# Kernel optimization log

Hardware: AMD Instinct MI355X
Metric: run time of the kernel (lower is better)

## Reference

```python
import jax, jax.numpy as jnp
import numpy as np

SHRINK_THRES = 0.0025
EPS = 1e-12  # F.normalize default eps


def _l2norm(v, axis=-1):
    return v / jnp.maximum(jnp.linalg.norm(v, axis=axis, keepdims=True), EPS)


def setup_inputs() -> dict:
    key = jax.random.key(0)
    ks = jax.random.split(key, 5)
    N, C, H, W = 16, 256, 64, 64
    mem_dim = 512
    x = jax.random.normal(ks[0], (N, C, H, W), dtype=jnp.float32)
    memory = jax.random.normal(ks[1], (mem_dim, C), dtype=jnp.float32) * 0.1
    memory = _l2norm(memory, axis=1)
    w1 = jax.random.normal(ks[2], (C, C // 2), dtype=jnp.float32) * (1.0 / np.sqrt(C))
    b1 = jnp.zeros((C // 2,), dtype=jnp.float32)
    w2 = jax.random.normal(ks[3], (C // 2, C), dtype=jnp.float32) * (1.0 / np.sqrt(C // 2))
    b2 = jnp.zeros((C,), dtype=jnp.float32)
    return {"x": x, "memory": memory, "w1": w1, "b1": b1, "w2": w2, "b2": b2}


def reference(x, memory, w1, b1, w2, b2):
    N, C, H, W = x.shape
    # [N,C,H,W] -> [N*H*W, C]
    x_flat = jnp.transpose(x, (0, 2, 3, 1)).reshape(-1, C)
    x_norm = _l2norm(x_flat, axis=1)
    # shared MLP over memory slots: Linear -> ReLU -> Linear -> ReLU
    m = jax.nn.relu(memory @ w1 + b1)
    m = jax.nn.relu(m @ w2 + b2)
    mem_norm = _l2norm(m, axis=1)  # [M, C]
    # cosine similarity + softmax over memory slots
    att = jax.nn.softmax(x_norm @ mem_norm.T, axis=1)  # [N*H*W, M]
    # hard shrink + L1 renormalization
    att = jax.nn.relu(att - SHRINK_THRES)
    att = att / jnp.maximum(jnp.sum(att, axis=1, keepdims=True), EPS)
    out_flat = att @ mem_norm  # [N*H*W, C]
    output = jnp.transpose(out_flat.reshape(N, H, W, C), (0, 3, 1, 2))
    att_map = jnp.transpose(att.reshape(N, H, W, -1), (0, 3, 1, 2))
    return output, att_map
```

## Files before the change

kernel.cpp:

```cpp
#include <hip/hip_runtime.h>
#include <hip/hip_bf16.h>

typedef _Float16 half8 __attribute__((ext_vector_type(8)));
typedef _Float16 half4v __attribute__((ext_vector_type(4)));
typedef float floatx4 __attribute__((ext_vector_type(4)));

#define C_DIM 256
#define M_DIM 512
#define HW 4096
#define TAU 0.0025f

__global__ __launch_bounds__(128) void prep_kernel(
    const float* __restrict__ memory, const float* __restrict__ w1,
    const float* __restrict__ b1, const float* __restrict__ w2,
    const float* __restrict__ b2,
    _Float16* __restrict__ mNh, _Float16* __restrict__ mNl,
    _Float16* __restrict__ mNt)
{
  __shared__ float sm[256];
  __shared__ float sh[128];
  __shared__ float s_part[2];
  __shared__ float s_tot;
  const int r = blockIdx.x;
  const int t = threadIdx.x;
  sm[t]       = memory[r * C_DIM + t];
  sm[t + 128] = memory[r * C_DIM + t + 128];
  __syncthreads();
  float acc = b1[t];
#pragma unroll 8
  for (int c = 0; c < 256; ++c) acc = fmaf(sm[c], w1[c * 128 + t], acc);
  sh[t] = fmaxf(acc, 0.f);
  __syncthreads();
  float o0 = b2[t], o1 = b2[t + 128];
#pragma unroll 8
  for (int k = 0; k < 128; ++k) {
    float h = sh[k];
    o0 = fmaf(h, w2[k * 256 + t], o0);
    o1 = fmaf(h, w2[k * 256 + t + 128], o1);
  }
  o0 = fmaxf(o0, 0.f);
  o1 = fmaxf(o1, 0.f);
  float ss = o0 * o0 + o1 * o1;
#pragma unroll
  for (int off = 32; off >= 1; off >>= 1) ss += __shfl_down(ss, off);
  if ((t & 63) == 0) s_part[t >> 6] = ss;
  __syncthreads();
  if (t == 0) s_tot = s_part[0] + s_part[1];
  __syncthreads();
  const float inv = 1.f / fmaxf(sqrtf(s_tot), 1e-12f);
  const float v0 = o0 * inv, v1 = o1 * inv;
  const _Float16 h0 = (_Float16)v0, h1 = (_Float16)v1;
  mNh[r * C_DIM + t]        = h0;
  mNh[r * C_DIM + t + 128]  = h1;
  mNl[r * C_DIM + t]        = (_Float16)(v0 - (float)h0);
  mNl[r * C_DIM + t + 128]  = (_Float16)(v1 - (float)h1);
  mNt[t * M_DIM + r]        = h0;
  mNt[(t + 128) * M_DIM + r] = h1;
}

__global__ __launch_bounds__(512, 2) void main_kernel(
    const float* __restrict__ x,
    const _Float16* __restrict__ mNh, const _Float16* __restrict__ mNl,
    const _Float16* __restrict__ mNt,
    float* __restrict__ out, float* __restrict__ attmap)
{
  __shared__ _Float16 Xh[64][264];
  __shared__ _Float16 Xl[64][264];
  __shared__ _Float16 attb[64][520];
  __shared__ float s_red[64][8];
  __shared__ float s_stat[64];
  __shared__ float s_inv[64];
  __shared__ float s_sumsq[64];

  const int tid  = threadIdx.x;
  const int wave = tid >> 6;
  const int lane = tid & 63;
  const int q    = lane >> 4;
  const int c16  = lane & 15;
  const int px   = tid & 63;
  const int g    = tid >> 6;

  const int blk = blockIdx.x;
  const int img = blk >> 6;
  const int hw0 = (blk & 63) * 64;
  const float* __restrict__ xb = x + (size_t)img * C_DIM * HW + hw0;

  if (tid < 64) s_sumsq[tid] = 0.f;
  __syncthreads();

  float part = 0.f;
#pragma unroll
  for (int i = 0; i < 8; ++i) {
    const int cb = i * 32 + g * 4;
    const float v0 = xb[(size_t)(cb + 0) * HW + px];
    const float v1 = xb[(size_t)(cb + 1) * HW + px];
    const float v2 = xb[(size_t)(cb + 2) * HW + px];
    const float v3 = xb[(size_t)(cb + 3) * HW + px];
    part += v0 * v0 + v1 * v1 + v2 * v2 + v3 * v3;
    const _Float16 h0 = (_Float16)v0, h1 = (_Float16)v1, h2 = (_Float16)v2, h3 = (_Float16)v3;
    half4v hv = {h0, h1, h2, h3};
    half4v lv = {(_Float16)(v0 - (float)h0), (_Float16)(v1 - (float)h1),
                 (_Float16)(v2 - (float)h2), (_Float16)(v3 - (float)h3)};
    *(half4v*)&Xh[px][cb] = hv;
    *(half4v*)&Xl[px][cb] = lv;
  }
  atomicAdd(&s_sumsq[px], part);
  __syncthreads();
  if (tid < 64) s_inv[tid] = 1.f / fmaxf(sqrtf(s_sumsq[tid]), 1e-12f);
  __syncthreads();

  floatx4 acc[4][4];
#pragma unroll
  for (int mt = 0; mt < 4; ++mt)
#pragma unroll
    for (int nt = 0; nt < 4; ++nt) {
      floatx4 z = {0.f, 0.f, 0.f, 0.f};
      acc[mt][nt] = z;
    }

#pragma unroll
  for (int kb = 0; kb < 8; ++kb) {
    const int k0 = kb * 32 + q * 8;
    half8 ah[4], al[4];
#pragma unroll
    for (int mt = 0; mt < 4; ++mt) {
      ah[mt] = *(const half8*)&Xh[mt * 16 + c16][k0];
      al[mt] = *(const half8*)&Xl[mt * 16 + c16][k0];
    }
#pragma unroll
    for (int nt = 0; nt < 4; ++nt) {
      const int n = wave * 64 + nt * 16 + c16;
      const half8 bh = *(const half8*)(mNh + (size_t)n * C_DIM + k0);
      const half8 bl = *(const half8*)(mNl + (size_t)n * C_DIM + k0);
#pragma unroll
      for (int mt = 0; mt < 4; ++mt) {
        acc[mt][nt] = __builtin_amdgcn_mfma_f32_16x16x32_f16(ah[mt], bh, acc[mt][nt], 0, 0, 0);
        acc[mt][nt] = __builtin_amdgcn_mfma_f32_16x16x32_f16(ah[mt], bl, acc[mt][nt], 0, 0, 0);
        acc[mt][nt] = __builtin_amdgcn_mfma_f32_16x16x32_f16(al[mt], bh, acc[mt][nt], 0, 0, 0);
      }
    }
  }

#pragma unroll
  for (int mt = 0; mt < 4; ++mt)
#pragma unroll
    for (int r = 0; r < 4; ++r) {
      const float iv = s_inv[mt * 16 + q * 4 + r];
#pragma unroll
      for (int nt = 0; nt < 4; ++nt) acc[mt][nt][r] *= iv;
    }

#pragma unroll
  for (int mt = 0; mt < 4; ++mt)
#pragma unroll
    for (int r = 0; r < 4; ++r) {
      float v = fmaxf(fmaxf(acc[mt][0][r], acc[mt][1][r]), fmaxf(acc[mt][2][r], acc[mt][3][r]));
      v = fmaxf(v, __shfl_xor(v, 1));
      v = fmaxf(v, __shfl_xor(v, 2));
      v = fmaxf(v, __shfl_xor(v, 4));
      v = fmaxf(v, __shfl_xor(v, 8));
      if (c16 == 0) s_red[mt * 16 + q * 4 + r][wave] = v;
    }
  __syncthreads();
  if (tid < 64) {
    float v = s_red[tid][0];
#pragma unroll
    for (int w = 1; w < 8; ++w) v = fmaxf(v, s_red[tid][w]);
    s_stat[tid] = v;
  }
  __syncthreads();

#pragma unroll
  for (int mt = 0; mt < 4; ++mt)
#pragma unroll
    for (int r = 0; r < 4; ++r) {
      const float mx = s_stat[mt * 16 + q * 4 + r];
      float s = 0.f;
#pragma unroll
      for (int nt = 0; nt < 4; ++nt) {
        const float e = __expf(acc[mt][nt][r] - mx);
        acc[mt][nt][r] = e;
        s += e;
      }
      s += __shfl_xor(s, 1);
      s += __shfl_xor(s, 2);
      s += __shfl_xor(s, 4);
      s += __shfl_xor(s, 8);
      if (c16 == 0) s_red[mt * 16 + q * 4 + r][wave] = s;
    }
  __syncthreads();
  if (tid < 64) {
    float v = 0.f;
#pragma unroll
    for (int w = 0; w < 8; ++w) v += s_red[tid][w];
    s_stat[tid] = 1.f / v;
  }
  __syncthreads();

#pragma unroll
  for (int mt = 0; mt < 4; ++mt)
#pragma unroll
    for (int r = 0; r < 4; ++r) {
      const float isum = s_stat[mt * 16 + q * 4 + r];
      float s = 0.f;
#pragma unroll
      for (int nt = 0; nt < 4; ++nt) {
        const float tv = fmaxf(acc[mt][nt][r] * isum - TAU, 0.f);
        acc[mt][nt][r] = tv;
        s += tv;
      }
      s += __shfl_xor(s, 1);
      s += __shfl_xor(s, 2);
      s += __shfl_xor(s, 4);
      s += __shfl_xor(s, 8);
      if (c16 == 0) s_red[mt * 16 + q * 4 + r][wave] = s;
    }
  __syncthreads();
  if (tid < 64) {
    float v = 0.f;
#pragma unroll
    for (int w = 0; w < 8; ++w) v += s_red[tid][w];
    s_stat[tid] = 1.f / fmaxf(v, 1e-12f);
  }
  __syncthreads();

#pragma unroll
  for (int mt = 0; mt < 4; ++mt)
#pragma unroll
    for (int r = 0; r < 4; ++r) {
      const int m = mt * 16 + q * 4 + r;
      const float rs = s_stat[m];
#pragma unroll
      for (int nt = 0; nt < 4; ++nt)
        attb[m][wave * 64 + nt * 16 + c16] = (_Float16)(acc[mt][nt][r] * rs);
    }
  __syncthreads();

#pragma unroll
  for (int i = 0; i < 16; ++i) {
    const int n0 = (g + 8 * i) * 4;
    const half4v v = *(const half4v*)&attb[px][n0];
    float* dst = attmap + ((size_t)img * M_DIM + n0) * HW + hw0 + px;
    dst[0]            = (float)v[0];
    dst[(size_t)HW]   = (float)v[1];
    dst[(size_t)2*HW] = (float)v[2];
    dst[(size_t)3*HW] = (float)v[3];
  }

  floatx4 acc2[4][2];
#pragma unroll
  for (int mt = 0; mt < 4; ++mt)
#pragma unroll
    for (int ct = 0; ct < 2; ++ct) {
      floatx4 z = {0.f, 0.f, 0.f, 0.f};
      acc2[mt][ct] = z;
    }
#pragma unroll
  for (int kb = 0; kb < 16; ++kb) {
    const int k0 = kb * 32 + q * 8;
    half8 a[4];
#pragma unroll
    for (int mt = 0; mt < 4; ++mt) a[mt] = *(const half8*)&attb[mt * 16 + c16][k0];
#pragma unroll
    for (int ct = 0; ct < 2; ++ct) {
      const int cc = wave * 32 + ct * 16 + c16;
      const half8 b = *(const half8*)(mNt + (size_t)cc * M_DIM + k0);
#pragma unroll
      for (int mt = 0; mt < 4; ++mt)
        acc2[mt][ct] = __builtin_amdgcn_mfma_f32_16x16x32_f16(a[mt], b, acc2[mt][ct], 0, 0, 0);
    }
  }

#pragma unroll
  for (int mt = 0; mt < 4; ++mt)
#pragma unroll
    for (int ct = 0; ct < 2; ++ct)
#pragma unroll
      for (int r = 0; r < 4; ++r)
        Xh[mt * 16 + q * 4 + r][wave * 32 + ct * 16 + c16] = (_Float16)acc2[mt][ct][r];
  __syncthreads();
#pragma unroll
  for (int i = 0; i < 8; ++i) {
    const int c0 = (g + 8 * i) * 4;
    const half4v v = *(const half4v*)&Xh[px][c0];
    float* dst = out + ((size_t)img * C_DIM + c0) * HW + hw0 + px;
    dst[0]            = (float)v[0];
    dst[(size_t)HW]   = (float)v[1];
    dst[(size_t)2*HW] = (float)v[2];
    dst[(size_t)3*HW] = (float)v[3];
  }
}

extern "C" void kernel_launch(void* const* d_in, const int* in_sizes, int n_in,
                              void* d_out, int out_size, void* d_ws, size_t ws_size,
                              hipStream_t stream) {
  (void)in_sizes; (void)n_in; (void)out_size; (void)ws_size;
  const float* x      = (const float*)d_in[0];
  const float* memory = (const float*)d_in[1];
  const float* w1     = (const float*)d_in[2];
  const float* b1     = (const float*)d_in[3];
  const float* w2     = (const float*)d_in[4];
  const float* b2     = (const float*)d_in[5];
  float* out    = (float*)d_out;
  float* attmap = out + (size_t)16 * C_DIM * HW;

  _Float16* mNh = (_Float16*)d_ws;
  _Float16* mNl = mNh + (size_t)M_DIM * C_DIM;
  _Float16* mNt = mNl + (size_t)M_DIM * C_DIM;

  hipLaunchKernelGGL(prep_kernel, dim3(M_DIM), dim3(128), 0, stream,
                     memory, w1, b1, w2, b2, mNh, mNl, mNt);
  hipLaunchKernelGGL(main_kernel, dim3(1024), dim3(512), 0, stream,
                     x, mNh, mNl, mNt, out, attmap);
}
```

Baseline: 395.6 us.

## Drop split-fp16 GEMM, skip softmax max, shrink tiles and alias shared memory

Removes the hi/lo fp16 split for x and memory, so the similarity GEMM uses one MFMA per tile instead of three. Drops the softmax max-subtraction pass, relying on cosine similarity being bounded in [-1,1]. Halves the pixel tile to 32 per block, doubling the grid, and aliases the X, attention and output buffers in one shared array so more blocks fit per CU (launch bounds raised). Output is staged as fp32 instead of fp16. The main risk is accuracy, since x is now only fp16 precision in the first GEMM.

```diff
diff --git a/kernel.cpp b/kernel.cpp
--- a/kernel.cpp
+++ b/kernel.cpp
@@ -14,8 +14,7 @@
     const float* __restrict__ memory, const float* __restrict__ w1,
     const float* __restrict__ b1, const float* __restrict__ w2,
     const float* __restrict__ b2,
-    _Float16* __restrict__ mNh, _Float16* __restrict__ mNl,
-    _Float16* __restrict__ mNt)
+    _Float16* __restrict__ mN, _Float16* __restrict__ mNt)
 {
   __shared__ float sm[256];
   __shared__ float sh[128];
@@ -50,68 +49,61 @@
   const float inv = 1.f / fmaxf(sqrtf(s_tot), 1e-12f);
   const float v0 = o0 * inv, v1 = o1 * inv;
   const _Float16 h0 = (_Float16)v0, h1 = (_Float16)v1;
-  mNh[r * C_DIM + t]        = h0;
-  mNh[r * C_DIM + t + 128]  = h1;
-  mNl[r * C_DIM + t]        = (_Float16)(v0 - (float)h0);
-  mNl[r * C_DIM + t + 128]  = (_Float16)(v1 - (float)h1);
+  mN[r * C_DIM + t]         = h0;
+  mN[r * C_DIM + t + 128]   = h1;
   mNt[t * M_DIM + r]        = h0;
   mNt[(t + 128) * M_DIM + r] = h1;
 }
 
-__global__ __launch_bounds__(512, 2) void main_kernel(
+__global__ __launch_bounds__(512, 6) void main_kernel(
     const float* __restrict__ x,
-    const _Float16* __restrict__ mNh, const _Float16* __restrict__ mNl,
+    const _Float16* __restrict__ mN,
     const _Float16* __restrict__ mNt,
     float* __restrict__ out, float* __restrict__ attmap)
 {
-  __shared__ _Float16 Xh[64][264];
-  __shared__ _Float16 Xl[64][264];
-  __shared__ _Float16 attb[64][520];
-  __shared__ float s_red[64][8];
-  __shared__ float s_stat[64];
-  __shared__ float s_inv[64];
-  __shared__ float s_sumsq[64];
+  __shared__ __align__(16) unsigned char smem_u[33280];
+  __shared__ float s_red[32][8];
+  __shared__ float s_stat[32];
+  __shared__ float s_sumsq[32];
+
+  _Float16 (*Xh)[264]   = (_Float16(*)[264])smem_u;
+  _Float16 (*attb)[520] = (_Float16(*)[520])smem_u;
+  float    (*Ost)[260]  = (float(*)[260])smem_u;
 
   const int tid  = threadIdx.x;
   const int wave = tid >> 6;
   const int lane = tid & 63;
   const int q    = lane >> 4;
   const int c16  = lane & 15;
-  const int px   = tid & 63;
-  const int g    = tid >> 6;
+  const int px   = tid & 31;
+  const int cg   = tid >> 5;
 
   const int blk = blockIdx.x;
-  const int img = blk >> 6;
-  const int hw0 = (blk & 63) * 64;
+  const int img = blk >> 7;
+  const int hw0 = (blk & 127) * 32;
   const float* __restrict__ xb = x + (size_t)img * C_DIM * HW + hw0;
 
-  if (tid < 64) s_sumsq[tid] = 0.f;
+  if (tid < 32) s_sumsq[tid] = 0.f;
   __syncthreads();
 
   float part = 0.f;
 #pragma unroll
-  for (int i = 0; i < 8; ++i) {
-    const int cb = i * 32 + g * 4;
+  for (int i = 0; i < 4; ++i) {
+    const int cb = i * 64 + cg * 4;
     const float v0 = xb[(size_t)(cb + 0) * HW + px];
     const float v1 = xb[(size_t)(cb + 1) * HW + px];
     const float v2 = xb[(size_t)(cb + 2) * HW + px];
     const float v3 = xb[(size_t)(cb + 3) * HW + px];
     part += v0 * v0 + v1 * v1 + v2 * v2 + v3 * v3;
-    const _Float16 h0 = (_Float16)v0, h1 = (_Float16)v1, h2 = (_Float16)v2, h3 = (_Float16)v3;
-    half4v hv = {h0, h1, h2, h3};
-    half4v lv = {(_Float16)(v0 - (float)h0), (_Float16)(v1 - (float)h1),
-                 (_Float16)(v2 - (float)h2), (_Float16)(v3 - (float)h3)};
+    half4v hv = {(_Float16)v0, (_Float16)v1, (_Float16)v2, (_Float16)v3};
     *(half4v*)&Xh[px][cb] = hv;
-    *(half4v*)&Xl[px][cb] = lv;
   }
   atomicAdd(&s_sumsq[px], part);
   __syncthreads();
-  if (tid < 64) s_inv[tid] = 1.f / fmaxf(sqrtf(s_sumsq[tid]), 1e-12f);
-  __syncthreads();
-
-  floatx4 acc[4][4];
-#pragma unroll
-  for (int mt = 0; mt < 4; ++mt)
+
+  floatx4 acc[2][4];
+#pragma unroll
+  for (int mt = 0; mt < 2; ++mt)
 #pragma unroll
     for (int nt = 0; nt < 4; ++nt) {
       floatx4 z = {0.f, 0.f, 0.f, 0.f};
@@ -121,64 +113,29 @@
 #pragma unroll
   for (int kb = 0; kb < 8; ++kb) {
     const int k0 = kb * 32 + q * 8;
-    half8 ah[4], al[4];
-#pragma unroll
-    for (int mt = 0; mt < 4; ++mt) {
-      ah[mt] = *(const half8*)&Xh[mt * 16 + c16][k0];
-      al[mt] = *(const half8*)&Xl[mt * 16 + c16][k0];
-    }
+    half8 ah[2];
+#pragma unroll
+    for (int mt = 0; mt < 2; ++mt) ah[mt] = *(const half8*)&Xh[mt * 16 + c16][k0];
 #pragma unroll
     for (int nt = 0; nt < 4; ++nt) {
       const int n = wave * 64 + nt * 16 + c16;
-      const half8 bh = *(const half8*)(mNh + (size_t)n * C_DIM + k0);
-      const half8 bl = *(const half8*)(mNl + (size_t)n * C_DIM + k0);
-#pragma unroll
-      for (int mt = 0; mt < 4; ++mt) {
+      const half8 bh = *(const half8*)(mN + (size_t)n * C_DIM + k0);
+#pragma unroll
+      for (int mt = 0; mt < 2; ++mt)
         acc[mt][nt] = __builtin_amdgcn_mfma_f32_16x16x32_f16(ah[mt], bh, acc[mt][nt], 0, 0, 0);
-        acc[mt][nt] = __builtin_amdgcn_mfma_f32_16x16x32_f16(ah[mt], bl, acc[mt][nt], 0, 0, 0);
-        acc[mt][nt] = __builtin_amdgcn_mfma_f32_16x16x32_f16(al[mt], bh, acc[mt][nt], 0, 0, 0);
-      }
-    }
-  }
-
-#pragma unroll
-  for (int mt = 0; mt < 4; ++mt)
+    }
+  }
+
+#pragma unroll
+  for (int mt = 0; mt < 2; ++mt)
 #pragma unroll
     for (int r = 0; r < 4; ++r) {
-      const float iv = s_inv[mt * 16 + q * 4 + r];
-#pragma unroll
-      for (int nt = 0; nt < 4; ++nt) acc[mt][nt][r] *= iv;
-    }
-
-#pragma unroll
-  for (int mt = 0; mt < 4; ++mt)
-#pragma unroll
-    for (int r = 0; r < 4; ++r) {
-      float v = fmaxf(fmaxf(acc[mt][0][r], acc[mt][1][r]), fmaxf(acc[mt][2][r], acc[mt][3][r]));
-      v = fmaxf(v, __shfl_xor(v, 1));
-      v = fmaxf(v, __shfl_xor(v, 2));
-      v = fmaxf(v, __shfl_xor(v, 4));
-      v = fmaxf(v, __shfl_xor(v, 8));
-      if (c16 == 0) s_red[mt * 16 + q * 4 + r][wave] = v;
-    }
-  __syncthreads();
-  if (tid < 64) {
-    float v = s_red[tid][0];
-#pragma unroll
-    for (int w = 1; w < 8; ++w) v = fmaxf(v, s_red[tid][w]);
-    s_stat[tid] = v;
-  }
-  __syncthreads();
-
-#pragma unroll
-  for (int mt = 0; mt < 4; ++mt)
-#pragma unroll
-    for (int r = 0; r < 4; ++r) {
-      const float mx = s_stat[mt * 16 + q * 4 + r];
+      const int m = mt * 16 + q * 4 + r;
+      const float iv = 1.f / fmaxf(sqrtf(s_sumsq[m]), 1e-12f);
       float s = 0.f;
 #pragma unroll
       for (int nt = 0; nt < 4; ++nt) {
-        const float e = __expf(acc[mt][nt][r] - mx);
+        const float e = __expf(acc[mt][nt][r] * iv);
         acc[mt][nt][r] = e;
         s += e;
       }
@@ -186,10 +143,10 @@
       s += __shfl_xor(s, 2);
       s += __shfl_xor(s, 4);
       s += __shfl_xor(s, 8);
-      if (c16 == 0) s_red[mt * 16 + q * 4 + r][wave] = s;
-    }
-  __syncthreads();
-  if (tid < 64) {
+      if (c16 == 0) s_red[m][wave] = s;
+    }
+  __syncthreads();
+  if (tid < 32) {
     float v = 0.f;
 #pragma unroll
     for (int w = 0; w < 8; ++w) v += s_red[tid][w];
@@ -198,10 +155,11 @@
   __syncthreads();
 
 #pragma unroll
-  for (int mt = 0; mt < 4; ++mt)
+  for (int mt = 0; mt < 2; ++mt)
 #pragma unroll
     for (int r = 0; r < 4; ++r) {
-      const float isum = s_stat[mt * 16 + q * 4 + r];
+      const int m = mt * 16 + q * 4 + r;
+      const float isum = s_stat[m];
       float s = 0.f;
 #pragma unroll
       for (int nt = 0; nt < 4; ++nt) {
@@ -213,10 +171,10 @@
       s += __shfl_xor(s, 2);
       s += __shfl_xor(s, 4);
       s += __shfl_xor(s, 8);
-      if (c16 == 0) s_red[mt * 16 + q * 4 + r][wave] = s;
-    }
-  __syncthreads();
-  if (tid < 64) {
+      if (c16 == 0) s_red[m][wave] = s;
+    }
+  __syncthreads();
+  if (tid < 32) {
     float v = 0.f;
 #pragma unroll
     for (int w = 0; w < 8; ++w) v += s_red[tid][w];
@@ -225,7 +183,7 @@
   __syncthreads();
 
 #pragma unroll
-  for (int mt = 0; mt < 4; ++mt)
+  for (int mt = 0; mt < 2; ++mt)
 #pragma unroll
     for (int r = 0; r < 4; ++r) {
       const int m = mt * 16 + q * 4 + r;
@@ -237,8 +195,8 @@
   __syncthreads();
 
 #pragma unroll
-  for (int i = 0; i < 16; ++i) {
-    const int n0 = (g + 8 * i) * 4;
+  for (int i = 0; i < 8; ++i) {
+    const int n0 = (cg + 16 * i) * 4;
     const half4v v = *(const half4v*)&attb[px][n0];
     float* dst = attmap + ((size_t)img * M_DIM + n0) * HW + hw0 + px;
     dst[0]            = (float)v[0];
@@ -247,9 +205,9 @@
     dst[(size_t)3*HW] = (float)v[3];
   }
 
-  floatx4 acc2[4][2];
-#pragma unroll
-  for (int mt = 0; mt < 4; ++mt)
+  floatx4 acc2[2][2];
+#pragma unroll
+  for (int mt = 0; mt < 2; ++mt)
 #pragma unroll
     for (int ct = 0; ct < 2; ++ct) {
       floatx4 z = {0.f, 0.f, 0.f, 0.f};
@@ -258,36 +216,37 @@
 #pragma unroll
   for (int kb = 0; kb < 16; ++kb) {
     const int k0 = kb * 32 + q * 8;
-    half8 a[4];
-#pragma unroll
-    for (int mt = 0; mt < 4; ++mt) a[mt] = *(const half8*)&attb[mt * 16 + c16][k0];
+    half8 a[2];
+#pragma unroll
+    for (int mt = 0; mt < 2; ++mt) a[mt] = *(const half8*)&attb[mt * 16 + c16][k0];
 #pragma unroll
     for (int ct = 0; ct < 2; ++ct) {
       const int cc = wave * 32 + ct * 16 + c16;
       const half8 b = *(const half8*)(mNt + (size_t)cc * M_DIM + k0);
 #pragma unroll
-      for (int mt = 0; mt < 4; ++mt)
+      for (int mt = 0; mt < 2; ++mt)
         acc2[mt][ct] = __builtin_amdgcn_mfma_f32_16x16x32_f16(a[mt], b, acc2[mt][ct], 0, 0, 0);
     }
   }
-
-#pragma unroll
-  for (int mt = 0; mt < 4; ++mt)
+  __syncthreads();
+
+#pragma unroll
+  for (int mt = 0; mt < 2; ++mt)
 #pragma unroll
     for (int ct = 0; ct < 2; ++ct)
 #pragma unroll
       for (int r = 0; r < 4; ++r)
-        Xh[mt * 16 + q * 4 + r][wave * 32 + ct * 16 + c16] = (_Float16)acc2[mt][ct][r];
-  __syncthreads();
-#pragma unroll
-  for (int i = 0; i < 8; ++i) {
-    const int c0 = (g + 8 * i) * 4;
-    const half4v v = *(const half4v*)&Xh[px][c0];
+        Ost[mt * 16 + q * 4 + r][wave * 32 + ct * 16 + c16] = acc2[mt][ct][r];
+  __syncthreads();
+#pragma unroll
+  for (int i = 0; i < 4; ++i) {
+    const int c0 = (cg + 16 * i) * 4;
+    const floatx4 v = *(const floatx4*)&Ost[px][c0];
     float* dst = out + ((size_t)img * C_DIM + c0) * HW + hw0 + px;
-    dst[0]            = (float)v[0];
-    dst[(size_t)HW]   = (float)v[1];
-    dst[(size_t)2*HW] = (float)v[2];
-    dst[(size_t)3*HW] = (float)v[3];
+    dst[0]            = v[0];
+    dst[(size_t)HW]   = v[1];
+    dst[(size_t)2*HW] = v[2];
+    dst[(size_t)3*HW] = v[3];
   }
 }
 
@@ -304,12 +263,11 @@
   float* out    = (float*)d_out;
   float* attmap = out + (size_t)16 * C_DIM * HW;
 
-  _Float16* mNh = (_Float16*)d_ws;
-  _Float16* mNl = mNh + (size_t)M_DIM * C_DIM;
-  _Float16* mNt = mNl + (size_t)M_DIM * C_DIM;
+  _Float16* mN  = (_Float16*)d_ws;
+  _Float16* mNt = mN + (size_t)M_DIM * C_DIM;
 
   hipLaunchKernelGGL(prep_kernel, dim3(M_DIM), dim3(128), 0, stream,
-                     memory, w1, b1, w2, b2, mNh, mNl, mNt);
-  hipLaunchKernelGGL(main_kernel, dim3(1024), dim3(512), 0, stream,
-                     x, mNh, mNl, mNt, out, attmap);
+                     memory, w1, b1, w2, b2, mN, mNt);
+  hipLaunchKernelGGL(main_kernel, dim3(2048), dim3(512), 0, stream,
+                     x, mN, mNt, out, attmap);
 }
```

After: 399.0 us. Within noise of the previous version (+0.8%).
